# Kernel optimization log

Hardware: AMD Instinct MI355X
Metric: run time of the kernel (lower is better)

The kernel has to match this reference:

```python
import jax, jax.numpy as jnp
import numpy as np

BATCH, L, IN_DIM, HID, STATE, MLP, OUT, NUM_LAYERS = 16, 2048, 64, 256, 256, 1024, 128, 4
MAX_PHASE = 2.0 * np.pi


def setup_inputs() -> dict:
    key = jax.random.key(0)
    ks = iter(jax.random.split(key, 32))
    x = jax.random.normal(next(ks), (BATCH, L, IN_DIM), dtype=jnp.float32)
    # embedding Linear(IN_DIM -> HID)
    emb_W = jax.random.normal(next(ks), (HID, IN_DIM), dtype=jnp.float32) / np.sqrt(IN_DIM)
    emb_b = jnp.zeros((HID,), dtype=jnp.float32)
    # LRU params per layer (r_min=0, r_max=1, max_phase=2pi)
    u1 = jax.random.uniform(next(ks), (NUM_LAYERS, STATE), minval=1e-4, maxval=1.0)
    u2 = jax.random.uniform(next(ks), (NUM_LAYERS, STATE), minval=1e-4, maxval=1.0)
    nu_log = jnp.log(-0.5 * jnp.log(u1))
    theta_log = jnp.log(MAX_PHASE * u2)
    lam_abs = jnp.exp(-jnp.exp(nu_log))
    gamma_log = jnp.log(jnp.sqrt(1.0 - lam_abs ** 2))
    B_re = jax.random.normal(next(ks), (NUM_LAYERS, STATE, HID)) / np.sqrt(2 * HID)
    B_im = jax.random.normal(next(ks), (NUM_LAYERS, STATE, HID)) / np.sqrt(2 * HID)
    C_re = jax.random.normal(next(ks), (NUM_LAYERS, HID, STATE)) / np.sqrt(STATE)
    C_im = jax.random.normal(next(ks), (NUM_LAYERS, HID, STATE)) / np.sqrt(STATE)
    D = jax.random.normal(next(ks), (NUM_LAYERS, HID))
    # block MLP: Linear(STATE->MLP), GELU, Linear(MLP->HID)
    Wh = jax.random.normal(next(ks), (NUM_LAYERS, MLP, STATE)) / np.sqrt(STATE)
    bh = jnp.zeros((NUM_LAYERS, MLP), dtype=jnp.float32)
    Wo = jax.random.normal(next(ks), (NUM_LAYERS, HID, MLP)) / np.sqrt(MLP)
    bo = jnp.zeros((NUM_LAYERS, HID), dtype=jnp.float32)
    # output Linear(HID -> OUT)
    out_W = jax.random.normal(next(ks), (OUT, HID), dtype=jnp.float32) / np.sqrt(HID)
    out_b = jnp.zeros((OUT,), dtype=jnp.float32)
    return {"x": x, "emb_W": emb_W, "emb_b": emb_b, "nu_log": nu_log,
            "theta_log": theta_log, "gamma_log": gamma_log, "B_re": B_re,
            "B_im": B_im, "C_re": C_re, "C_im": C_im, "D": D,
            "Wh": Wh, "bh": bh, "Wo": Wo, "bo": bo,
            "out_W": out_W, "out_b": out_b}


def _binop(ei, ej):
    a_i, bu_i = ei
    a_j, bu_j = ej
    return a_j * a_i, a_j * bu_i + bu_j


def _lru(x, nu, th, gl, Bre, Bim, Cre, Cim, D):
    # x: (B, L, H) real; state diag recurrence in complex64
    lam = jnp.exp(-jnp.exp(nu) + 1j * jnp.exp(th))               # (S,)
    B_norm = (Bre + 1j * Bim) * jnp.exp(gl)[:, None]             # (S, H)
    Bu = jnp.einsum("blh,sh->bls", x.astype(B_norm.dtype), B_norm)  # (B, L, S)
    Lam = jnp.broadcast_to(lam, Bu.shape)
    _, states = jax.lax.associative_scan(_binop, (Lam, Bu), axis=1)
    C = Cre + 1j * Cim                                           # (H, S)
    y = jnp.einsum("bls,hs->blh", states, C).real + D * x        # (B, L, H)
    return y


def reference(x, emb_W, emb_b, nu_log, theta_log, gamma_log, B_re, B_im,
              C_re, C_im, D, Wh, bh, Wo, bo, out_W, out_b):
    h = x @ emb_W.T + emb_b                                      # (B, L, HID)
    for l in range(NUM_LAYERS):
        y = _lru(h, nu_log[l], theta_log[l], gamma_log[l],
                 B_re[l], B_im[l], C_re[l], C_im[l], D[l])
        z = jax.nn.gelu(y @ Wh[l].T + bh[l], approximate=False)  # exact GELU as torch
        h = z @ Wo[l].T + bo[l] + y                              # residual
    return h @ out_W.T + out_b                                   # (B, L, OUT)
```

## Files before the change

### kernel.cpp

```cpp
#include <hip/hip_runtime.h>
#include <hip/hip_bf16.h>
#include <math.h>

typedef __hip_bfloat16 bf16;
typedef __attribute__((ext_vector_type(8))) short bf16x8;
typedef __attribute__((ext_vector_type(4))) float f32x4;

#define BATCH   16
#define SEQLEN  2048
#define INDIM   64
#define HIDD    256
#define STATE_D 256
#define MLPD    1024
#define OUTD    128
#define NLAYERS 4
#define M_TOK   (BATCH*SEQLEN)
#define CHUNK   64
#define NCHUNK  (SEQLEN/CHUNK)

__device__ float g_carry[512*512];
__device__ bf16  g_hb [(size_t)M_TOK*256];
__device__ bf16  g_yb [(size_t)M_TOK*256];
__device__ bf16  g_bub[(size_t)M_TOK*512];
__device__ bf16  g_Bnb[NLAYERS*512*256];
__device__ bf16  g_Cwb[NLAYERS*256*512];
__device__ bf16  g_Whb[NLAYERS*1024*256];
__device__ bf16  g_Wob[NLAYERS*256*1024];

#define SB_HB  0
#define SB_YB  1
#define SB_BUB 2
#define SB_BNB 4
#define SB_CWB 5
#define SB_WHB 6
#define SB_WOB 7

__device__ __forceinline__ bf16* bufb(int sel){
  switch(sel){
    case SB_HB:  return g_hb;  case SB_YB:  return g_yb;
    case SB_BUB: return g_bub;
    case SB_BNB: return g_Bnb; case SB_CWB: return g_Cwb;
    case SB_WHB: return g_Whb; default:     return g_Wob; }
}

__device__ __forceinline__ void gld_lds16(const void* g, void* l){
  __builtin_amdgcn_global_load_lds(
      (const __attribute__((address_space(1))) unsigned int*)g,
      (__attribute__((address_space(3))) unsigned int*)l, 16, 0, 0);
}

__device__ __forceinline__ float fast_gelu(float v){
  const float x  = v * 0.70710678118654752f;
  const float ax = fabsf(x);
  const float t  = __builtin_amdgcn_rcpf(fmaf(0.3275911f, ax, 1.0f));
  float p = fmaf(t, 1.061405429f, -1.453152027f);
  p = fmaf(t, p, 1.421413741f);
  p = fmaf(t, p, -0.284496736f);
  p = fmaf(t, p, 0.254829592f);
  p = p * t;
  const float e = __expf(-ax * ax);
  const float erf_ax = fmaf(-p, e, 1.0f);
  const float erf_x  = copysignf(erf_ax, x);
  return 0.5f * v * (1.0f + erf_x);
}

__device__ __forceinline__ unsigned int bf2_add(unsigned int a, unsigned int b){
  float alo = __uint_as_float(a << 16), ahi = __uint_as_float(a & 0xffff0000u);
  float blo = __uint_as_float(b << 16), bhi = __uint_as_float(b & 0xffff0000u);
  bf16 l = __float2bfloat16(alo + blo);
  bf16 h = __float2bfloat16(ahi + bhi);
  return (unsigned int)(*reinterpret_cast<unsigned short*>(&l))
       | ((unsigned int)(*reinterpret_cast<unsigned short*>(&h)) << 16);
}

__device__ __forceinline__ void lam_of(const float* __restrict__ nu_log,
                                       const float* __restrict__ th_log,
                                       int s, float& lr, float& li)
{
  float nu  = expf(nu_log[s]);
  float th  = expf(th_log[s]);
  float mag = expf(-nu);
  lr = mag * cosf(th);
  li = mag * sinf(th);
}

#define RPSTR 136

template<int ACT, int FLAGS>
__global__ __launch_bounds__(256, 6) void mfma_gemm(
    int aSel, int lda, int wSel, int wOff, int ldw,
    int oSel, int ldc,
    const float* __restrict__ bias,
    int rSel, int ldres,
    const float* __restrict__ dscale,
    int K,
    const float* __restrict__ nu_log,
    const float* __restrict__ th_log)
{
  const bf16* A = bufb(aSel);
  const bf16* W = bufb(wSel) + wOff;
  bf16* OB = bufb(oSel);
  const bf16* res = (rSel >= 0) ? bufb(rSel) : nullptr;

  __shared__ __align__(16) unsigned short lds[12288];
  unsigned short* As = lds;
  unsigned short* Ws = lds + 4096;

  const int gx = gridDim.x;
  const int nwg = gx * gridDim.y;
  const int orig = blockIdx.y * gx + blockIdx.x;
  const int q = nwg >> 3, r = nwg & 7;
  const int xcd = orig & 7, idx = orig >> 3;
  const int wg = (xcd < r ? xcd*(q+1) : r*(q+1) + (xcd-r)*q) + idx;
  const int bx = wg % gx, by = wg / gx;

  const int tid  = threadIdx.x;
  const int row0 = by * 64, col0 = bx * 128;
  const int lane = tid & 63;
  const int m16  = lane & 15, quad = lane >> 4;
  const int wv   = tid >> 6;
  const int wm   = (wv & 1) * 32, wn = (wv >> 1) * 64;

  const int rlo = wv*16 + (lane >> 2);
  const int sg  = ((lane & 3) ^ ((rlo >> 1) & 3)) * 8;
  const bf16* ga = &A[(size_t)(row0 + rlo)*lda + sg];
  const bf16* gw = &W[(size_t)(col0 + rlo)*ldw + sg];
  const size_t w64 = (size_t)64 * ldw;

  auto STAGE = [&](int bb, int k0){
    unsigned short* Ab = As + bb*2048;
    unsigned short* Wb = Ws + bb*4096;
    gld_lds16(ga + k0,       Ab + wv*512);
    gld_lds16(gw + k0,       Wb + wv*512);
    gld_lds16(gw + k0 + w64, Wb + 2048 + wv*512);
  };

  f32x4 acc[2][4] = {};
  const int nt = K >> 5;

  STAGE(0, 0); STAGE(1, 32);

  for (int t = 0; t < nt; ++t){
    const int b = t & 1;
    if (t + 1 < nt) asm volatile("s_waitcnt vmcnt(3)" ::: "memory");
    else            asm volatile("s_waitcnt vmcnt(0)" ::: "memory");
    __builtin_amdgcn_s_barrier();

    const unsigned short* Ab = As + b*2048;
    const unsigned short* Wb = Ws + b*4096;
    bf16x8 af[2], wf[4];
    #pragma unroll
    for (int i = 0; i < 2; i++){
      const int rA = wm + 16*i + m16;
      af[i] = *reinterpret_cast<const bf16x8*>(&Ab[rA*32 + ((quad ^ ((rA>>1)&3))<<3)]);
    }
    #pragma unroll
    for (int j = 0; j < 4; j++){
      const int rW = wn + 16*j + m16;
      wf[j] = *reinterpret_cast<const bf16x8*>(&Wb[rW*32 + ((quad ^ ((rW>>1)&3))<<3)]);
    }
    asm volatile("s_waitcnt lgkmcnt(0)" ::: "memory");
    __builtin_amdgcn_sched_barrier(0);
    __builtin_amdgcn_s_barrier();

    if (t + 2 < nt) STAGE(b, (t + 2) << 5);

    __builtin_amdgcn_s_setprio(1);
    #pragma unroll
    for (int i = 0; i < 2; i++)
      #pragma unroll
      for (int j = 0; j < 4; j++)
        acc[i][j] = __builtin_amdgcn_mfma_f32_16x16x32_bf16(af[i], wf[j], acc[i][j], 0, 0, 0);
    __builtin_amdgcn_s_setprio(0);
  }

  #pragma unroll
  for (int i = 0; i < 2; i++){
    #pragma unroll
    for (int j = 0; j < 4; j++){
      const int lcol = wn + 16*j + m16;
      const int col  = col0 + lcol;
      #pragma unroll
      for (int r2 = 0; r2 < 4; r2++){
        const int lrow = wm + 16*i + quad*4 + r2;
        const int row  = row0 + lrow;
        float v = acc[i][j][r2];
        if (FLAGS & 1) v += bias[col];
        if (ACT == 1)  v = fast_gelu(v);
        if (FLAGS & 2) v += __bfloat162float(res[(size_t)row*ldres + col]);
        if (FLAGS & 4) v += dscale[col] * __bfloat162float(res[(size_t)row*ldres + col]);
        bf16 bv = __float2bfloat16(v);
        lds[lrow*RPSTR + lcol] = *reinterpret_cast<unsigned short*>(&bv);
      }
    }
  }
  __syncthreads();

  {
    const int rr  = tid >> 4;
    const int c16 = (tid & 15) * 8;
    #pragma unroll
    for (int s = 0; s < 4; s++){
      const int orow = s*16 + rr;
      uint4 d = *reinterpret_cast<const uint4*>(&lds[orow*RPSTR + c16]);
      *reinterpret_cast<uint4*>(OB + (size_t)(row0 + orow)*ldc + col0 + c16) = d;
    }
  }

  if (FLAGS & 8){
    if (tid < 64){
      const int sglob = (col0 >> 1) + tid;
      float lr, li; lam_of(nu_log, th_log, sglob, lr, li);
      float ar = 0.f, ai = 0.f;
      for (int t = 0; t < CHUNK; t++){
        unsigned int pr = *reinterpret_cast<const unsigned int*>(&lds[t*RPSTR + 2*tid]);
        float br = __uint_as_float(pr << 16);
        float bi = __uint_as_float(pr & 0xffff0000u);
        float nr = fmaf(lr, ar, fmaf(-li, ai, br));
        float ni = fmaf(lr, ai, fmaf( li, ar, bi));
        ar = nr; ai = ni;
      }
      g_carry[(size_t)by*512 + 2*sglob]     = ar;
      g_carry[(size_t)by*512 + 2*sglob + 1] = ai;
    }
  }
}

__global__ __launch_bounds__(256, 2) void fused_mlp(
    int whOff, int woOff,
    const float* __restrict__ bh, const float* __restrict__ bo)
{
  const bf16* Wh = g_Whb + whOff;
  const bf16* Wo = g_Wob + woOff;

  __shared__ __align__(16) unsigned short As[2*2048];
  __shared__ __align__(16) unsigned short Ws[2*8192];
  __shared__ __align__(16) unsigned short zbuf[64*132];

  const int tid  = threadIdx.x;
  const int row0 = blockIdx.x * 64;
  const int lane = tid & 63;
  const int m16  = lane & 15, quad = lane >> 4;
  const int wv   = tid >> 6;
  const int wm   = (wv & 1) * 32;
  const int wnA  = (wv >> 1) * 64;
  const int wnB  = (wv >> 1) * 128;

  const int rlo = wv*16 + (lane >> 2);
  const int sg  = ((lane & 3) ^ ((rlo >> 1) & 3)) * 8;

  const bf16* ga = g_yb + (size_t)(row0 + rlo)*HIDD + sg;

  f32x4 accB[2][8] = {};

  for (int mc = 0; mc < 8; ++mc){
    const bf16* gwh = Wh + (size_t)(mc*128 + rlo)*HIDD + sg;
    const bf16* gwo = Wo + (size_t)rlo*MLPD + mc*128 + sg;

    auto STAGE_A = [&](int b, int k0){
      gld_lds16(ga + k0,            As + b*2048 + wv*512);
      gld_lds16(gwh + k0,           Ws + b*8192 + wv*512);
      gld_lds16(gwh + k0 + 64*HIDD, Ws + b*8192 + 2048 + wv*512);
    };
    auto STAGE_B = [&](int b, int ks){
      const bf16* src = gwo + ks*32;
      #pragma unroll
      for (int g = 0; g < 4; g++)
        gld_lds16(src + (size_t)g*64*MLPD, Ws + b*8192 + g*2048 + wv*512);
    };

    f32x4 accA[2][4] = {};
    STAGE_A(0, 0); STAGE_A(1, 32);
    for (int t = 0; t < 8; ++t){
      const int b = t & 1;
      if (t + 1 < 8) asm volatile("s_waitcnt vmcnt(3)" ::: "memory");
      else           asm volatile("s_waitcnt vmcnt(0)" ::: "memory");
      __builtin_amdgcn_s_barrier();
      const unsigned short* Ab = As + b*2048;
      const unsigned short* Wb = Ws + b*8192;
      bf16x8 af[2], wf[4];
      #pragma unroll
      for (int i = 0; i < 2; i++){
        const int rA = wm + 16*i + m16;
        af[i] = *reinterpret_cast<const bf16x8*>(&Ab[rA*32 + ((quad ^ ((rA>>1)&3))<<3)]);
      }
      #pragma unroll
      for (int j = 0; j < 4; j++){
        const int rW = wnA + 16*j + m16;
        wf[j] = *reinterpret_cast<const bf16x8*>(&Wb[rW*32 + ((quad ^ ((rW>>1)&3))<<3)]);
      }
      asm volatile("s_waitcnt lgkmcnt(0)" ::: "memory");
      __builtin_amdgcn_sched_barrier(0);
      __builtin_amdgcn_s_barrier();
      if (t + 2 < 8) STAGE_A(b, (t + 2) << 5);
      __builtin_amdgcn_s_setprio(1);
      #pragma unroll
      for (int i = 0; i < 2; i++)
        #pragma unroll
        for (int j = 0; j < 4; j++)
          accA[i][j] = __builtin_amdgcn_mfma_f32_16x16x32_bf16(af[i], wf[j], accA[i][j], 0, 0, 0);
      __builtin_amdgcn_s_setprio(0);
    }
    STAGE_B(0, 0); STAGE_B(1, 1);

    #pragma unroll
    for (int i = 0; i < 2; i++){
      #pragma unroll
      for (int j = 0; j < 4; j++){
        const int lcol = wnA + 16*j + m16;
        const float bb = bh[mc*128 + lcol];
        #pragma unroll
        for (int r2 = 0; r2 < 4; r2++){
          const int lrow = wm + 16*i + quad*4 + r2;
          float v = fast_gelu(accA[i][j][r2] + bb);
          bf16 bv = __float2bfloat16(v);
          zbuf[lrow*132 + lcol] = *reinterpret_cast<unsigned short*>(&bv);
        }
      }
    }
    __syncthreads();

    for (int ks = 0; ks < 4; ++ks){
      const int b = ks & 1;
      if (ks + 1 < 4) asm volatile("s_waitcnt vmcnt(4)" ::: "memory");
      else            asm volatile("s_waitcnt vmcnt(0)" ::: "memory");
      __builtin_amdgcn_s_barrier();
      const unsigned short* Wb = Ws + b*8192;
      bf16x8 af[2], wf[8];
      #pragma unroll
      for (int i = 0; i < 2; i++){
        const int rA = wm + 16*i + m16;
        af[i] = *reinterpret_cast<const bf16x8*>(&zbuf[rA*132 + ks*32 + quad*8]);
      }
      #pragma unroll
      for (int j = 0; j < 8; j++){
        const int rW = wnB + 16*j + m16;
        wf[j] = *reinterpret_cast<const bf16x8*>(&Wb[rW*32 + ((quad ^ ((rW>>1)&3))<<3)]);
      }
      asm volatile("s_waitcnt lgkmcnt(0)" ::: "memory");
      __builtin_amdgcn_sched_barrier(0);
      __builtin_amdgcn_s_barrier();
      if (ks + 2 < 4) STAGE_B(b, ks + 2);
      __builtin_amdgcn_s_setprio(1);
      #pragma unroll
      for (int i = 0; i < 2; i++)
        #pragma unroll
        for (int j = 0; j < 8; j++)
          accB[i][j] = __builtin_amdgcn_mfma_f32_16x16x32_bf16(af[i], wf[j], accB[i][j], 0, 0, 0);
      __builtin_amdgcn_s_setprio(0);
    }
  }

  #pragma unroll
  for (int n = 0; n < 2; n++){
    __syncthreads();
    if ((wv >> 1) == n){
      #pragma unroll
      for (int i = 0; i < 2; i++){
        #pragma unroll
        for (int j = 0; j < 8; j++){
          const int lcol = 16*j + m16;
          const float bb = bo[n*128 + lcol];
          #pragma unroll
          for (int r2 = 0; r2 < 4; r2++){
            const int lrow = wm + 16*i + quad*4 + r2;
            float v = accB[i][j][r2] + bb;
            bf16 bv = __float2bfloat16(v);
            zbuf[lrow*132 + lcol] = *reinterpret_cast<unsigned short*>(&bv);
          }
        }
      }
    }
    __syncthreads();
    const int rr = tid >> 4, c16 = (tid & 15) * 8;
    #pragma unroll
    for (int s = 0; s < 4; s++){
      const int orow = s*16 + rr;
      uint4 hv = *reinterpret_cast<const uint4*>(&zbuf[orow*132 + c16]);
      const size_t go = (size_t)(row0 + orow)*HIDD + n*128 + c16;
      uint4 yv = *reinterpret_cast<const uint4*>(g_yb + go);
      uint4 o;
      o.x = bf2_add(hv.x, yv.x); o.y = bf2_add(hv.y, yv.y);
      o.z = bf2_add(hv.z, yv.z); o.w = bf2_add(hv.w, yv.w);
      *reinterpret_cast<uint4*>(g_hb + go) = o;
    }
  }
}

__global__ __launch_bounds__(256) void emb_gemm(
    const float* __restrict__ x, const float* __restrict__ W,
    const float* __restrict__ b)
{
  __shared__ __align__(16) float Asx[16][68];
  __shared__ __align__(16) float Wsx[16][68];
  const int tid = threadIdx.x;
  const int tx = tid & 15, ty = tid >> 4;
  const int row0 = blockIdx.y * 64, col0 = blockIdx.x * 64;
  const int lc = tid & 15, lr = tid >> 4;
  float acc[4][4] = {};
  for (int k0 = 0; k0 < INDIM; k0 += 16){
    #pragma unroll
    for (int i = 0; i < 4; i++){
      Asx[lc][lr + 16*i] = x[(size_t)(row0 + lr + 16*i)*INDIM + k0 + lc];
      Wsx[lc][lr + 16*i] = W[(size_t)(col0 + lr + 16*i)*INDIM + k0 + lc];
    }
    __syncthreads();
    #pragma unroll
    for (int k = 0; k < 16; k++){
      float4 av = *reinterpret_cast<const float4*>(&Asx[k][ty*4]);
      float4 bv = *reinterpret_cast<const float4*>(&Wsx[k][tx*4]);
      float a[4] = {av.x, av.y, av.z, av.w};
      float b2[4] = {bv.x, bv.y, bv.z, bv.w};
      #pragma unroll
      for (int i = 0; i < 4; i++)
        #pragma unroll
        for (int j = 0; j < 4; j++)
          acc[i][j] = fmaf(a[i], b2[j], acc[i][j]);
    }
    __syncthreads();
  }
  #pragma unroll
  for (int i = 0; i < 4; i++){
    const int r = row0 + ty*4 + i;
    #pragma unroll
    for (int j = 0; j < 4; j++){
      const int cn = col0 + tx*4 + j;
      g_hb[(size_t)r*HIDD + cn] = __float2bfloat16(acc[i][j] + b[cn]);
    }
  }
}

__global__ __launch_bounds__(256) void out_gemm(
    const float* __restrict__ W, const float* __restrict__ b,
    float* __restrict__ out)
{
  __shared__ __align__(16) float Asx[16][68];
  __shared__ __align__(16) float Wsx[16][68];
  const int tid = threadIdx.x;
  const int tx = tid & 15, ty = tid >> 4;
  const int row0 = blockIdx.y * 64, col0 = blockIdx.x * 64;
  const int lc = tid & 15, lr = tid >> 4;
  float acc[4][4] = {};
  for (int k0 = 0; k0 < HIDD; k0 += 16){
    #pragma unroll
    for (int i = 0; i < 4; i++){
      Asx[lc][lr + 16*i] = __bfloat162float(g_hb[(size_t)(row0 + lr + 16*i)*HIDD + k0 + lc]);
      Wsx[lc][lr + 16*i] = W[(size_t)(col0 + lr + 16*i)*HIDD + k0 + lc];
    }
    __syncthreads();
    #pragma unroll
    for (int k = 0; k < 16; k++){
      float4 av = *reinterpret_cast<const float4*>(&Asx[k][ty*4]);
      float4 bv = *reinterpret_cast<const float4*>(&Wsx[k][tx*4]);
      float a[4] = {av.x, av.y, av.z, av.w};
      float b2[4] = {bv.x, bv.y, bv.z, bv.w};
      #pragma unroll
      for (int i = 0; i < 4; i++)
        #pragma unroll
        for (int j = 0; j < 4; j++)
          acc[i][j] = fmaf(a[i], b2[j], acc[i][j]);
    }
    __syncthreads();
  }
  #pragma unroll
  for (int i = 0; i < 4; i++){
    const int r = row0 + ty*4 + i;
    #pragma unroll
    for (int j = 0; j < 4; j++){
      const int cn = col0 + tx*4 + j;
      out[(size_t)r*OUTD + cn] = acc[i][j] + b[cn];
    }
  }
}

__global__ __launch_bounds__(256) void scan_fix(
    const float* __restrict__ nu_log, const float* __restrict__ th_log)
{
  const int blk = blockIdx.x;
  const int c   = blk & (NCHUNK - 1);
  const int s   = threadIdx.x;
  float lr, li; lam_of(nu_log, th_log, s, lr, li);
  float cr = 0.f, ci = 0.f;
  if (c > 0){
    float Tr = lr, Ti = li;
    #pragma unroll
    for (int i = 0; i < 6; i++){ float nr = Tr*Tr - Ti*Ti; Ti = 2.f*Tr*Ti; Tr = nr; }
    const int bstart = blk - c;
    for (int j = 0; j < c; j++){
      float2 e = *reinterpret_cast<const float2*>(&g_carry[(size_t)(bstart + j)*512 + 2*s]);
      float nr = fmaf(Tr, cr, fmaf(-Ti, ci, e.x));
      float ni = fmaf(Tr, ci, fmaf( Ti, cr, e.y));
      cr = nr; ci = ni;
    }
  }
  float ar = cr, ai = ci;
  unsigned int* pb = reinterpret_cast<unsigned int*>(g_bub) + (size_t)blk*CHUNK*256 + s;
  for (int t = 0; t < CHUNK; t++){
    unsigned int pr = pb[(size_t)t*256];
    float br = __uint_as_float(pr << 16);
    float bi = __uint_as_float(pr & 0xffff0000u);
    float nr = fmaf(lr, ar, fmaf(-li, ai, br));
    float ni = fmaf(lr, ai, fmaf( li, ar, bi));
    ar = nr; ai = ni;
    bf16 hr = __float2bfloat16(ar), hi2 = __float2bfloat16(ai);
    unsigned int w = (unsigned int)(*reinterpret_cast<unsigned short*>(&hr))
                   | ((unsigned int)(*reinterpret_cast<unsigned short*>(&hi2)) << 16);
    pb[(size_t)t*256] = w;
  }
}

__global__ __launch_bounds__(256) void pack_B(
    const float* __restrict__ Bre, const float* __restrict__ Bim,
    const float* __restrict__ gl)
{
  int idx = blockIdx.x * 256 + threadIdx.x;
  int l = idx >> 16, within = idx & 65535;
  int s = within >> 8, h = within & 255;
  float g = expf(gl[l*STATE_D + s]);
  g_Bnb[(size_t)l*131072 + (size_t)(2*s  )*256 + h] = __float2bfloat16(Bre[idx] * g);
  g_Bnb[(size_t)l*131072 + (size_t)(2*s+1)*256 + h] = __float2bfloat16(Bim[idx] * g);
}

__global__ __launch_bounds__(256) void pack_C(
    const float* __restrict__ Cre, const float* __restrict__ Cim)
{
  int idx = blockIdx.x * 256 + threadIdx.x;
  int l = idx >> 16, within = idx & 65535;
  int h = within >> 8, s = within & 255;
  g_Cwb[(size_t)l*131072 + (size_t)h*512 + 2*s]     = __float2bfloat16( Cre[idx]);
  g_Cwb[(size_t)l*131072 + (size_t)h*512 + 2*s + 1] = __float2bfloat16(-Cim[idx]);
}

__global__ __launch_bounds__(256) void conv_bf16(
    const float* __restrict__ src, int dstSel, int n)
{
  int i = blockIdx.x * 256 + threadIdx.x;
  if (i < n) bufb(dstSel)[i] = __float2bfloat16(src[i]);
}

extern "C" void kernel_launch(void* const* d_in, const int* in_sizes, int n_in,
                              void* d_out, int out_size, void* d_ws, size_t ws_size,
                              hipStream_t stream)
{
  (void)d_ws; (void)ws_size; (void)out_size; (void)n_in; (void)in_sizes;
  const float* x      = (const float*)d_in[0];
  const float* emb_W  = (const float*)d_in[1];
  const float* emb_b  = (const float*)d_in[2];
  const float* nu_log = (const float*)d_in[3];
  const float* th_log = (const float*)d_in[4];
  const float* ga_log = (const float*)d_in[5];
  const float* B_re   = (const float*)d_in[6];
  const float* B_im   = (const float*)d_in[7];
  const float* C_re   = (const float*)d_in[8];
  const float* C_im   = (const float*)d_in[9];
  const float* Dv     = (const float*)d_in[10];
  const float* Wh     = (const float*)d_in[11];
  const float* bh     = (const float*)d_in[12];
  const float* Wo     = (const float*)d_in[13];
  const float* bo     = (const float*)d_in[14];
  const float* out_W  = (const float*)d_in[15];
  const float* out_b  = (const float*)d_in[16];

  const dim3 blk(256);

  pack_B<<<dim3(NLAYERS*256), blk, 0, stream>>>(B_re, B_im, ga_log);
  pack_C<<<dim3(NLAYERS*256), blk, 0, stream>>>(C_re, C_im);
  conv_bf16<<<dim3(NLAYERS*1024), blk, 0, stream>>>(Wh, SB_WHB, NLAYERS*262144);
  conv_bf16<<<dim3(NLAYERS*1024), blk, 0, stream>>>(Wo, SB_WOB, NLAYERS*262144);

  emb_gemm<<<dim3(HIDD/64, M_TOK/64), blk, 0, stream>>>(x, emb_W, emb_b);

  for (int l = 0; l < NLAYERS; l++){
    mfma_gemm<0, 8><<<dim3(4, M_TOK/64), blk, 0, stream>>>(
        SB_HB, HIDD, SB_BNB, l*131072, HIDD, SB_BUB, 512,
        nullptr, -1, 0, nullptr, HIDD,
        nu_log + l*STATE_D, th_log + l*STATE_D);

    scan_fix<<<dim3(M_TOK/CHUNK), blk, 0, stream>>>(nu_log + l*STATE_D, th_log + l*STATE_D);

    mfma_gemm<0, 4><<<dim3(2, M_TOK/64), blk, 0, stream>>>(
        SB_BUB, 512, SB_CWB, l*131072, 512, SB_YB, HIDD,
        nullptr, SB_HB, HIDD, Dv + l*HIDD, 512, nullptr, nullptr);

    fused_mlp<<<dim3(M_TOK/64), blk, 0, stream>>>(
        l*262144, l*262144, bh + l*MLPD, bo + l*HIDD);
  }

  out_gemm<<<dim3(OUTD/64, M_TOK/64), blk, 0, stream>>>(out_W, out_b, (float*)d_out);
}
```

Before: 751.7 us.

## Run fused MLP kernel with 512 threads and smaller per-wave tiles

The fused MLP kernel moves from 4 to 8 waves per block. Each wave now computes a 16-row slice instead of 32 rows, which halves the accumulator register arrays, and the staging loads are redistributed so each wave issues fewer global-to-LDS copies. Full __syncthreads are replaced with explicit lgkmcnt waits and raw s_barriers. The aim is more waves in flight to hide latency, at the cost of less A-fragment reuse per wave and more barrier participants.

```diff
diff --git a/kernel.cpp b/kernel.cpp
--- a/kernel.cpp
+++ b/kernel.cpp
@@ -226,7 +226,7 @@
   }
 }
 
-__global__ __launch_bounds__(256, 2) void fused_mlp(
+__global__ __launch_bounds__(512, 4) void fused_mlp(
     int whOff, int woOff,
     const float* __restrict__ bh, const float* __restrict__ bo)
 {
@@ -242,48 +242,46 @@
   const int lane = tid & 63;
   const int m16  = lane & 15, quad = lane >> 4;
   const int wv   = tid >> 6;
-  const int wm   = (wv & 1) * 32;
-  const int wnA  = (wv >> 1) * 64;
-  const int wnB  = (wv >> 1) * 128;
-
-  const int rlo = wv*16 + (lane >> 2);
-  const int sg  = ((lane & 3) ^ ((rlo >> 1) & 3)) * 8;
-
-  const bf16* ga = g_yb + (size_t)(row0 + rlo)*HIDD + sg;
-
-  f32x4 accB[2][8] = {};
+  const int wm   = (wv & 3) * 16;
+  const int wnA  = (wv >> 2) * 64;
+  const int wnB  = (wv >> 2) * 128;
+
+  const int lsub = lane >> 2;
+  const int rloA = (wv & 3) * 16 + lsub;
+  const int sgA  = ((lane & 3) ^ ((rloA >> 1) & 3)) * 8;
+  const int rloW = wv * 16 + lsub;
+  const int sgW  = ((lane & 3) ^ ((rloW >> 1) & 3)) * 8;
+
+  const bf16* ga = g_yb + (size_t)(row0 + rloA)*HIDD + sgA;
+
+  f32x4 accB[8] = {};
 
   for (int mc = 0; mc < 8; ++mc){
-    const bf16* gwh = Wh + (size_t)(mc*128 + rlo)*HIDD + sg;
-    const bf16* gwo = Wo + (size_t)rlo*MLPD + mc*128 + sg;
+    const bf16* gwh = Wh + (size_t)(mc*128 + rloW)*HIDD + sgW;
 
     auto STAGE_A = [&](int b, int k0){
-      gld_lds16(ga + k0,            As + b*2048 + wv*512);
-      gld_lds16(gwh + k0,           Ws + b*8192 + wv*512);
-      gld_lds16(gwh + k0 + 64*HIDD, Ws + b*8192 + 2048 + wv*512);
+      gld_lds16(ga + k0,  As + b*2048 + (wv & 3)*512);
+      gld_lds16(gwh + k0, Ws + b*8192 + wv*512);
     };
     auto STAGE_B = [&](int b, int ks){
-      const bf16* src = gwo + ks*32;
-      #pragma unroll
-      for (int g = 0; g < 4; g++)
-        gld_lds16(src + (size_t)g*64*MLPD, Ws + b*8192 + g*2048 + wv*512);
+      #pragma unroll
+      for (int g = 0; g < 2; g++)
+        gld_lds16(Wo + (size_t)(g*128 + rloW)*MLPD + mc*128 + ks*32 + sgW,
+                  Ws + b*8192 + g*4096 + wv*512);
     };
 
-    f32x4 accA[2][4] = {};
+    f32x4 accA[4] = {};
     STAGE_A(0, 0); STAGE_A(1, 32);
     for (int t = 0; t < 8; ++t){
       const int b = t & 1;
-      if (t + 1 < 8) asm volatile("s_waitcnt vmcnt(3)" ::: "memory");
+      if (t + 1 < 8) asm volatile("s_waitcnt vmcnt(2)" ::: "memory");
       else           asm volatile("s_waitcnt vmcnt(0)" ::: "memory");
       __builtin_amdgcn_s_barrier();
       const unsigned short* Ab = As + b*2048;
       const unsigned short* Wb = Ws + b*8192;
-      bf16x8 af[2], wf[4];
-      #pragma unroll
-      for (int i = 0; i < 2; i++){
-        const int rA = wm + 16*i + m16;
-        af[i] = *reinterpret_cast<const bf16x8*>(&Ab[rA*32 + ((quad ^ ((rA>>1)&3))<<3)]);
-      }
+      bf16x8 af, wf[4];
+      { const int rA = wm + m16;
+        af = *reinterpret_cast<const bf16x8*>(&Ab[rA*32 + ((quad ^ ((rA>>1)&3))<<3)]); }
       #pragma unroll
       for (int j = 0; j < 4; j++){
         const int rW = wnA + 16*j + m16;
@@ -295,43 +293,39 @@
       if (t + 2 < 8) STAGE_A(b, (t + 2) << 5);
       __builtin_amdgcn_s_setprio(1);
       #pragma unroll
-      for (int i = 0; i < 2; i++)
-        #pragma unroll
-        for (int j = 0; j < 4; j++)
-          accA[i][j] = __builtin_amdgcn_mfma_f32_16x16x32_bf16(af[i], wf[j], accA[i][j], 0, 0, 0);
+      for (int j = 0; j < 4; j++)
+        accA[j] = __builtin_amdgcn_mfma_f32_16x16x32_bf16(af, wf[j], accA[j], 0, 0, 0);
       __builtin_amdgcn_s_setprio(0);
     }
+
     STAGE_B(0, 0); STAGE_B(1, 1);
 
     #pragma unroll
-    for (int i = 0; i < 2; i++){
-      #pragma unroll
-      for (int j = 0; j < 4; j++){
-        const int lcol = wnA + 16*j + m16;
-        const float bb = bh[mc*128 + lcol];
-        #pragma unroll
-        for (int r2 = 0; r2 < 4; r2++){
-          const int lrow = wm + 16*i + quad*4 + r2;
-          float v = fast_gelu(accA[i][j][r2] + bb);
-          bf16 bv = __float2bfloat16(v);
-          zbuf[lrow*132 + lcol] = *reinterpret_cast<unsigned short*>(&bv);
-        }
+    for (int j = 0; j < 4; j++){
+      const int lcol = wnA + 16*j + m16;
+      const float bb = bh[mc*128 + lcol];
+      #pragma unroll
+      for (int r2 = 0; r2 < 4; r2++){
+        const int lrow = wm + quad*4 + r2;
+        float v = fast_gelu(accA[j][r2] + bb);
+        bf16 bv = __float2bfloat16(v);
+        zbuf[lrow*132 + lcol] = *reinterpret_cast<unsigned short*>(&bv);
       }
     }
-    __syncthreads();
+    asm volatile("s_waitcnt lgkmcnt(0)" ::: "memory");
+    __builtin_amdgcn_sched_barrier(0);
+    __builtin_amdgcn_s_barrier();
+    __builtin_amdgcn_sched_barrier(0);
 
     for (int ks = 0; ks < 4; ++ks){
       const int b = ks & 1;
-      if (ks + 1 < 4) asm volatile("s_waitcnt vmcnt(4)" ::: "memory");
+      if (ks + 1 < 4) asm volatile("s_waitcnt vmcnt(2)" ::: "memory");
       else            asm volatile("s_waitcnt vmcnt(0)" ::: "memory");
       __builtin_amdgcn_s_barrier();
       const unsigned short* Wb = Ws + b*8192;
-      bf16x8 af[2], wf[8];
-      #pragma unroll
-      for (int i = 0; i < 2; i++){
-        const int rA = wm + 16*i + m16;
-        af[i] = *reinterpret_cast<const bf16x8*>(&zbuf[rA*132 + ks*32 + quad*8]);
-      }
+      bf16x8 af, wf[8];
+      { const int rA = wm + m16;
+        af = *reinterpret_cast<const bf16x8*>(&zbuf[rA*132 + ks*32 + quad*8]); }
       #pragma unroll
       for (int j = 0; j < 8; j++){
         const int rW = wnB + 16*j + m16;
@@ -343,39 +337,40 @@
       if (ks + 2 < 4) STAGE_B(b, ks + 2);
       __builtin_amdgcn_s_setprio(1);
       #pragma unroll
-      for (int i = 0; i < 2; i++)
-        #pragma unroll
-        for (int j = 0; j < 8; j++)
-          accB[i][j] = __builtin_amdgcn_mfma_f32_16x16x32_bf16(af[i], wf[j], accB[i][j], 0, 0, 0);
+      for (int j = 0; j < 8; j++)
+        accB[j] = __builtin_amdgcn_mfma_f32_16x16x32_bf16(af, wf[j], accB[j], 0, 0, 0);
       __builtin_amdgcn_s_setprio(0);
     }
   }
 
   #pragma unroll
   for (int n = 0; n < 2; n++){
-    __syncthreads();
-    if ((wv >> 1) == n){
-      #pragma unroll
-      for (int i = 0; i < 2; i++){
+    asm volatile("s_waitcnt lgkmcnt(0)" ::: "memory");
+    __builtin_amdgcn_sched_barrier(0);
+    __builtin_amdgcn_s_barrier();
+    __builtin_amdgcn_sched_barrier(0);
+    if ((wv >> 2) == n){
+      #pragma unroll
+      for (int j = 0; j < 8; j++){
+        const int lcol = 16*j + m16;
+        const float bb = bo[n*128 + lcol];
         #pragma unroll
-        for (int j = 0; j < 8; j++){
-          const int lcol = 16*j + m16;
-          const float bb = bo[n*128 + lcol];
-          #pragma unroll
-          for (int r2 = 0; r2 < 4; r2++){
-            const int lrow = wm + 16*i + quad*4 + r2;
-            float v = accB[i][j][r2] + bb;
-            bf16 bv = __float2bfloat16(v);
-            zbuf[lrow*132 + lcol] = *reinterpret_cast<unsigned short*>(&bv);
-          }
+        for (int r2 = 0; r2 < 4; r2++){
+          const int lrow = wm + quad*4 + r2;
+          float v = accB[j][r2] + bb;
+          bf16 bv = __float2bfloat16(v);
+          zbuf[lrow*132 + lcol] = *reinterpret_cast<unsigned short*>(&bv);
         }
       }
     }
-    __syncthreads();
+    asm volatile("s_waitcnt lgkmcnt(0)" ::: "memory");
+    __builtin_amdgcn_sched_barrier(0);
+    __builtin_amdgcn_s_barrier();
+    __builtin_amdgcn_sched_barrier(0);
     const int rr = tid >> 4, c16 = (tid & 15) * 8;
     #pragma unroll
-    for (int s = 0; s < 4; s++){
-      const int orow = s*16 + rr;
+    for (int s = 0; s < 2; s++){
+      const int orow = s*32 + rr;
       uint4 hv = *reinterpret_cast<const uint4*>(&zbuf[orow*132 + c16]);
       const size_t go = (size_t)(row0 + orow)*HIDD + n*128 + c16;
       uint4 yv = *reinterpret_cast<const uint4*>(g_yb + go);
@@ -582,7 +577,7 @@
         SB_BUB, 512, SB_CWB, l*131072, 512, SB_YB, HIDD,
         nullptr, SB_HB, HIDD, Dv + l*HIDD, 512, nullptr, nullptr);
 
-    fused_mlp<<<dim3(M_TOK/64), blk, 0, stream>>>(
+    fused_mlp<<<dim3(M_TOK/64), dim3(512), 0, stream>>>(
         l*262144, l*262144, bh + l*MLPD, bo + l*HIDD);
   }
 
```

After: 767.7 us. 1.02x slower.
